# Kernel optimization log

Hardware: AMD Instinct MI355X
Metric: run time of the kernel (lower is better)

## Reference

```python
import jax, jax.numpy as jnp
import numpy as np

B, T, D = 4, 512, 128
HID = 64
INIT = 0.02


def setup_inputs() -> dict:
    key = jax.random.key(0)
    ks = jax.random.split(key, 8)
    h = jax.random.normal(ks[0], (B, T, D), dtype=jnp.float32)
    h_src = jax.random.normal(ks[1], (B, T, D), dtype=jnp.float32)
    # Linear weights stored as (in, out); init std matches cfg.v_phi_init_scale, biases zero.
    W1 = jax.random.normal(ks[2], (3 * D, HID), dtype=jnp.float32) * INIT
    b1 = jnp.zeros((HID,), dtype=jnp.float32)
    W2 = jax.random.normal(ks[3], (HID, HID), dtype=jnp.float32) * INIT
    b2 = jnp.zeros((HID,), dtype=jnp.float32)
    W3 = jax.random.normal(ks[4], (HID, 1), dtype=jnp.float32) * INIT
    b3 = jnp.zeros((1,), dtype=jnp.float32)
    return {"h": h, "h_src": h_src, "W1": W1, "b1": b1, "W2": W2, "b2": b2, "W3": W3, "b3": b3}


def reference(h, h_src, W1, b1, W2, b2, W3, b3):
    # feats = cat(h_q, h_k, h_q - h_k) @ W1  ==  h_q @ (W1q + W1d) + h_k @ (W1k - W1d)
    # This avoids materializing the (B,T,T,3D) concat tensor while computing identical math.
    W1q, W1k, W1d = W1[:D], W1[D:2 * D], W1[2 * D:]
    pq = jnp.einsum('btd,dh->bth', h, W1q + W1d)        # (B,T,HID)
    pk = jnp.einsum('bsd,dh->bsh', h_src, W1k - W1d)    # (B,T,HID)
    x = jax.nn.gelu(pq[:, :, None, :] + pk[:, None, :, :] + b1, approximate=False)  # (B,T,T,HID)
    x = jax.nn.gelu(jnp.einsum('btsh,hk->btsk', x, W2) + b2, approximate=False)
    out = jnp.einsum('btsh,ho->btso', x, W3) + b3       # (B,T,T,1)
    return out[..., 0]                                   # (B,T,T)
```

## Files before the change

### kernel.cpp

```cpp
#include <hip/hip_runtime.h>

#define BB 4
#define TT 512
#define SS 512
#define DD 128
#define HID 64

typedef _Float16 f16;
typedef f16 f16x4 __attribute__((ext_vector_type(4)));
typedef f16 f16x8 __attribute__((ext_vector_type(8)));
typedef float f32x4 __attribute__((ext_vector_type(4)));

#define SPLAT8(c) ((f16x8){(f16)(c),(f16)(c),(f16)(c),(f16)(c),(f16)(c),(f16)(c),(f16)(c),(f16)(c)})

__device__ __forceinline__ f16x8 gelu_h(f16x8 xh) {
    f16x8 v = xh * xh;
    f16x8 p = __builtin_elementwise_fma(v, SPLAT8(-7.84424e-3f), SPLAT8(6.836736e-2f));
    p = __builtin_elementwise_fma(p, v, SPLAT8(-2.6470144e-1f));
    p = __builtin_elementwise_fma(p, v, SPLAT8(6.286528e-1f));
    p = __builtin_elementwise_fma(p, v, SPLAT8(-1.0660912f));
    p = __builtin_elementwise_fma(p, v, SPLAT8(1.596200f));
    return __builtin_elementwise_fma(v, p, xh);
}

__global__ __launch_bounds__(256) void pqk_kernel(
    const float* __restrict__ h, const float* __restrict__ h_src,
    const float* __restrict__ W1, const float* __restrict__ b1,
    const float* __restrict__ W2, const float* __restrict__ b2,
    const float* __restrict__ W3, const float* __restrict__ b3,
    f16* __restrict__ pq, f16* __restrict__ pk,
    f16* __restrict__ w3q, f16* __restrict__ betaq,
    float* __restrict__ clvp)
{
    if (blockIdx.x == 64) {
        const int t = threadIdx.x;
        if (t < HID) {
            const int kh2 = t >> 5, rem = t & 31;
            const int gg  = rem >> 3, ii = rem & 7;
            const int n   = (kh2 * 2 + (ii >> 2)) * 16 + gg * 4 + (ii & 3);
            w3q[t]   = (f16)(0.39894228f * W3[n]);
            betaq[t] = (f16)fmaf(2.0f, b2[n], 1.25331414f);
        } else if (t == HID) {
            float cl = b3[0];
            for (int n = 0; n < HID; ++n)
                cl = fmaf(W3[n], fmaf(0.39894228f * b2[n], b2[n], 0.5f * b2[n]), cl);
            clvp[0] = cl;
        }
        return;
    }

    const int tid  = threadIdx.x;
    const int wave = tid >> 6;
    const int lane = tid & 63;
    const int g = lane >> 4;
    const int r = lane & 15;

    const int half = blockIdx.x >> 5;
    const int row0 = (blockIdx.x & 31) * 64 + wave * 16;

    const float* src = half ? h_src : h;
    const float* Wa  = W1 + (half ? DD * HID : 0);
    const float* Wd  = W1 + 2 * DD * HID;
    const float  sgn = half ? -1.0f : 1.0f;
    f16* dst = half ? pk : pq;

    f16x8 aw[4][4];
    #pragma unroll
    for (int ks = 0; ks < 4; ++ks) {
        #pragma unroll
        for (int nb = 0; nb < 4; ++nb) {
            const float* wa = Wa + (ks * 32 + g * 8) * HID + nb * 16 + r;
            const float* wd = Wd + (ks * 32 + g * 8) * HID + nb * 16 + r;
            f16x8 v;
            #pragma unroll
            for (int i = 0; i < 8; ++i)
                v[i] = (f16)fmaf(sgn, wd[i * HID], wa[i * HID]);
            aw[ks][nb] = v;
        }
    }

    f16x8 bx[4];
    const float* srow = src + (size_t)(row0 + r) * DD + g * 8;
    #pragma unroll
    for (int ks = 0; ks < 4; ++ks) {
        float4 q0 = *(const float4*)(srow + ks * 32);
        float4 q1 = *(const float4*)(srow + ks * 32 + 4);
        f16x8 v;
        v[0] = (f16)q0.x; v[1] = (f16)q0.y; v[2] = (f16)q0.z; v[3] = (f16)q0.w;
        v[4] = (f16)q1.x; v[5] = (f16)q1.y; v[6] = (f16)q1.z; v[7] = (f16)q1.w;
        bx[ks] = v;
    }

    #pragma unroll
    for (int nb = 0; nb < 4; ++nb) {
        f32x4 acc;
        if (half == 0) {
            float4 bv = *(const float4*)(b1 + nb * 16 + g * 4);
            acc = (f32x4){bv.x, bv.y, bv.z, bv.w};
        } else {
            acc = (f32x4){0.f, 0.f, 0.f, 0.f};
        }
        #pragma unroll
        for (int ks = 0; ks < 4; ++ks)
            acc = __builtin_amdgcn_mfma_f32_16x16x32_f16(aw[ks][nb], bx[ks], acc, 0, 0, 0);
        f16x4 w;
        w[0] = (f16)acc[0]; w[1] = (f16)acc[1];
        w[2] = (f16)acc[2]; w[3] = (f16)acc[3];
        *(f16x4*)(dst + (size_t)(row0 + r) * HID + nb * 16 + g * 4) = w;
    }
}

#define LOADKV(KV0, KV1, CHUNK) {                                         \
    const f16* p_ = pkbase + (size_t)(CHUNK) * 16 * HID;                  \
    (KV0) = *(const f16x8*)(p_);                                          \
    (KV1) = *(const f16x8*)(p_ + 32); }

#define STAGE1(KV0, KV1) {                                                \
    a0 = gelu_h(__builtin_elementwise_fma((KV0), SPLAT8(0.5f), pqh0));    \
    a1 = gelu_h(__builtin_elementwise_fma((KV1), SPLAT8(0.5f), pqh1)); }

#define DOMFMA(ACC) {                                                     \
    _Pragma("unroll")                                                     \
    for (int nb = 0; nb < 4; ++nb) {                                      \
        ACC[nb] = __builtin_amdgcn_mfma_f32_16x16x32_f16(bw[0][nb], a0, Z4, 0, 0, 0); \
        ACC[nb] = __builtin_amdgcn_mfma_f32_16x16x32_f16(bw[1][nb], a1, ACC[nb], 0, 0, 0); \
    } }

#define STAGE2(ACC, C) {                                                  \
    f16x8 z0, z1;                                                         \
    _Pragma("unroll")                                                     \
    for (int i = 0; i < 8; ++i) {                                         \
        z0[i] = (f16)ACC[i >> 2][i & 3];                                  \
        z1[i] = (f16)ACC[2 + (i >> 2)][i & 3];                            \
    }                                                                     \
    z0 = z0 * (z0 + betaA0);                                              \
    z1 = z1 * (z1 + betaA1);                                              \
    f32x4 accQ = __builtin_amdgcn_mfma_f32_16x16x32_f16(w3qA0, z0, Z4, 0, 0, 0); \
    accQ = __builtin_amdgcn_mfma_f32_16x16x32_f16(w3qA1, z1, accQ, 0, 0, 0); \
    if (lane < 16) orow[(C) * 16 + lane] = accQ[0] + clv; }

__global__ __launch_bounds__(256, 4) void main_kernel(
    const f16* __restrict__ pq, const f16* __restrict__ pk,
    const float* __restrict__ W2,
    const f16* __restrict__ w3q, const f16* __restrict__ betaq,
    const float* __restrict__ clvp, float* __restrict__ out)
{
    const int tid  = threadIdx.x;
    const int wave = tid >> 6;
    const int lane = tid & 63;
    const int g = lane >> 4;
    const int r = lane & 15;

    const int wu  = blockIdx.x * 4 + wave;
    const int bt  = wu >> 2;
    const int sb0 = (wu & 3) * 128;
    const int b   = bt >> 9;

    f16x8 bw[2][4];
    #pragma unroll
    for (int kh = 0; kh < 2; ++kh) {
        #pragma unroll
        for (int nb = 0; nb < 4; ++nb) {
            const float* src = W2 + (kh * 32 + g * 8) * HID + nb * 16 + r;
            f16x8 v;
            #pragma unroll
            for (int i = 0; i < 8; ++i) v[i] = (f16)src[i * HID];
            bw[kh][nb] = v;
        }
    }

    const f16* pqrow = pq + (size_t)bt * HID + g * 8;
    f16x8 pqh0 = (*(const f16x8*)(pqrow)) * SPLAT8(0.5f);
    f16x8 pqh1 = (*(const f16x8*)(pqrow + 32)) * SPLAT8(0.5f);

    f16x8 w3qA0  = *(const f16x8*)(w3q + g * 8);
    f16x8 w3qA1  = *(const f16x8*)(w3q + 32 + g * 8);
    f16x8 betaA0 = *(const f16x8*)(betaq + g * 8);
    f16x8 betaA1 = *(const f16x8*)(betaq + 32 + g * 8);

    const float clv = clvp[0];
    const f32x4 Z4 = {0.f, 0.f, 0.f, 0.f};

    const f16* pkbase = pk + ((size_t)b * SS + sb0 + r) * HID + g * 8;
    float* orow = out + (size_t)bt * SS + sb0;

    f16x8 kvA0, kvA1, kvB0, kvB1;
    f16x8 a0, a1;
    f32x4 accA[4], accB[4];

    LOADKV(kvA0, kvA1, 0)
    LOADKV(kvB0, kvB1, 1)
    STAGE1(kvA0, kvA1)
    DOMFMA(accA)
    LOADKV(kvA0, kvA1, 2)
    STAGE1(kvB0, kvB1)
    DOMFMA(accB)

    #pragma unroll
    for (int cc = 0; cc < 3; ++cc) {
        LOADKV(kvB0, kvB1, 2 * cc + 3)
        STAGE1(kvA0, kvA1)
        STAGE2(accA, 2 * cc)
        DOMFMA(accA)
        if (cc < 2) LOADKV(kvA0, kvA1, 2 * cc + 4)
        STAGE1(kvB0, kvB1)
        STAGE2(accB, 2 * cc + 1)
        DOMFMA(accB)
    }
    STAGE2(accA, 6)
    STAGE2(accB, 7)
}

extern "C" void kernel_launch(void* const* d_in, const int* in_sizes, int n_in,
                              void* d_out, int out_size, void* d_ws, size_t ws_size,
                              hipStream_t stream) {
    const float* h     = (const float*)d_in[0];
    const float* h_src = (const float*)d_in[1];
    const float* W1    = (const float*)d_in[2];
    const float* b1    = (const float*)d_in[3];
    const float* W2    = (const float*)d_in[4];
    const float* b2    = (const float*)d_in[5];
    const float* W3    = (const float*)d_in[6];
    const float* b3    = (const float*)d_in[7];
    float* out = (float*)d_out;

    f16* pq    = (f16*)d_ws;
    f16* pk    = pq + (size_t)BB * TT * HID;
    f16* w3q   = pk + (size_t)BB * SS * HID;
    f16* betaq = w3q + HID;
    float* clvp = (float*)(betaq + HID);

    pqk_kernel<<<65, 256, 0, stream>>>(h, h_src, W1, b1, W2, b2, W3, b3,
                                       pq, pk, w3q, betaq, clvp);
    main_kernel<<<BB * TT * (SS / 128) / 4, 256, 0, stream>>>(pq, pk, W2,
                                                              w3q, betaq, clvp, out);
}
```

Baseline: 33.25 us.

## Prepack W2 to f16 fragments and double per-wave s-range with single accumulator

The prep kernel now converts W2 once into an f16 MFMA-fragment layout, so each main-kernel wave loads its B operands with eight vector loads instead of 64 strided fp32 loads and conversions. Each wave now covers 256 source positions instead of 128, halving the grid to 1024 blocks so the W2, pq, w3 and beta setup is amortised over twice the work. The two-accumulator ping-pong becomes a single accumulator inside an 8-iteration unrolled loop, which frees registers but serialises the MFMA and GELU stages more tightly. Fewer blocks also means less parallelism to hide latency.

```diff
diff --git a/kernel.cpp b/kernel.cpp
--- a/kernel.cpp
+++ b/kernel.cpp
@@ -29,11 +29,22 @@
     const float* __restrict__ W2, const float* __restrict__ b2,
     const float* __restrict__ W3, const float* __restrict__ b3,
     f16* __restrict__ pq, f16* __restrict__ pk,
-    f16* __restrict__ w3q, f16* __restrict__ betaq,
-    float* __restrict__ clvp)
+    f16* __restrict__ w2f, f16* __restrict__ w3q,
+    f16* __restrict__ betaq, float* __restrict__ clvp)
 {
     if (blockIdx.x == 64) {
         const int t = threadIdx.x;
+        #pragma unroll
+        for (int j = 0; j < 16; ++j) {
+            const int idx  = t * 16 + j;
+            const int kh   = idx >> 11;
+            const int nb   = (idx >> 9) & 3;
+            const int lane = (idx >> 3) & 63;
+            const int i    = idx & 7;
+            const int k    = kh * 32 + (lane >> 4) * 8 + i;
+            const int n    = nb * 16 + (lane & 15);
+            w2f[idx] = (f16)W2[k * HID + n];
+        }
         if (t < HID) {
             const int kh2 = t >> 5, rem = t & 31;
             const int gg  = rem >> 3, ii = rem & 7;
@@ -141,7 +152,7 @@
 
 __global__ __launch_bounds__(256, 4) void main_kernel(
     const f16* __restrict__ pq, const f16* __restrict__ pk,
-    const float* __restrict__ W2,
+    const f16* __restrict__ w2f,
     const f16* __restrict__ w3q, const f16* __restrict__ betaq,
     const float* __restrict__ clvp, float* __restrict__ out)
 {
@@ -152,22 +163,16 @@
     const int r = lane & 15;
 
     const int wu  = blockIdx.x * 4 + wave;
-    const int bt  = wu >> 2;
-    const int sb0 = (wu & 3) * 128;
+    const int bt  = wu >> 1;
+    const int sb0 = (wu & 1) * 256;
     const int b   = bt >> 9;
 
     f16x8 bw[2][4];
     #pragma unroll
-    for (int kh = 0; kh < 2; ++kh) {
-        #pragma unroll
-        for (int nb = 0; nb < 4; ++nb) {
-            const float* src = W2 + (kh * 32 + g * 8) * HID + nb * 16 + r;
-            f16x8 v;
-            #pragma unroll
-            for (int i = 0; i < 8; ++i) v[i] = (f16)src[i * HID];
-            bw[kh][nb] = v;
-        }
-    }
+    for (int kh = 0; kh < 2; ++kh)
+        #pragma unroll
+        for (int nb = 0; nb < 4; ++nb)
+            bw[kh][nb] = *(const f16x8*)(w2f + ((kh * 4 + nb) * 64 + lane) * 8);
 
     const f16* pqrow = pq + (size_t)bt * HID + g * 8;
     f16x8 pqh0 = (*(const f16x8*)(pqrow)) * SPLAT8(0.5f);
@@ -186,29 +191,26 @@
 
     f16x8 kvA0, kvA1, kvB0, kvB1;
     f16x8 a0, a1;
-    f32x4 accA[4], accB[4];
+    f32x4 acc[4];
 
     LOADKV(kvA0, kvA1, 0)
     LOADKV(kvB0, kvB1, 1)
     STAGE1(kvA0, kvA1)
-    DOMFMA(accA)
-    LOADKV(kvA0, kvA1, 2)
-    STAGE1(kvB0, kvB1)
-    DOMFMA(accB)
-
-    #pragma unroll
-    for (int cc = 0; cc < 3; ++cc) {
-        LOADKV(kvB0, kvB1, 2 * cc + 3)
-        STAGE1(kvA0, kvA1)
-        STAGE2(accA, 2 * cc)
-        DOMFMA(accA)
-        if (cc < 2) LOADKV(kvA0, kvA1, 2 * cc + 4)
+
+    #pragma unroll
+    for (int cc = 0; cc < 8; ++cc) {
+        DOMFMA(acc)
+        if (cc < 7) LOADKV(kvA0, kvA1, 2 * cc + 2)
         STAGE1(kvB0, kvB1)
-        STAGE2(accB, 2 * cc + 1)
-        DOMFMA(accB)
-    }
-    STAGE2(accA, 6)
-    STAGE2(accB, 7)
+        STAGE2(acc, 2 * cc)
+
+        DOMFMA(acc)
+        if (cc < 7) {
+            LOADKV(kvB0, kvB1, 2 * cc + 3)
+            STAGE1(kvA0, kvA1)
+        }
+        STAGE2(acc, 2 * cc + 1)
+    }
 }
 
 extern "C" void kernel_launch(void* const* d_in, const int* in_sizes, int n_in,
@@ -226,12 +228,12 @@
 
     f16* pq    = (f16*)d_ws;
     f16* pk    = pq + (size_t)BB * TT * HID;
-    f16* w3q   = pk + (size_t)BB * SS * HID;
+    f16* w2f   = pk + (size_t)BB * SS * HID;
+    f16* w3q   = w2f + HID * HID;
     f16* betaq = w3q + HID;
     float* clvp = (float*)(betaq + HID);
 
     pqk_kernel<<<65, 256, 0, stream>>>(h, h_src, W1, b1, W2, b2, W3, b3,
-                                       pq, pk, w3q, betaq, clvp);
-    main_kernel<<<BB * TT * (SS / 128) / 4, 256, 0, stream>>>(pq, pk, W2,
-                                                              w3q, betaq, clvp, out);
-}
+                                       pq, pk, w2f, w3q, betaq, clvp);
+    main_kernel<<<1024, 256, 0, stream>>>(pq, pk, w2f, w3q, betaq, clvp, out);
+}
```

After: 29.50 us. 11.3% less time.
